# Performance work log

Measured on AMD Instinct MI355X. Metric: run time of the kernel, lower is better.

The kernel has to match this reference:

```python
import jax, jax.numpy as jnp
import numpy as np

DT = 10.0 / 200  # 0.05
DX = 20.0 / 128  # 0.15625

# 5x5 fixed finite-difference stencils (torch Conv2d = cross-correlation, so use as-is)
_LAPL = np.array([[0, 0, -1/12, 0, 0],
                  [0, 0,  4/3,  0, 0],
                  [-1/12, 4/3, -5, 4/3, -1/12],
                  [0, 0,  4/3,  0, 0],
                  [0, 0, -1/12, 0, 0]], dtype=np.float32)
_PAR_X = np.array([[0, 0,  1/12, 0, 0],
                   [0, 0, -8/12, 0, 0],
                   [0, 0,  0,    0, 0],
                   [0, 0,  8/12, 0, 0],
                   [0, 0, -1/12, 0, 0]], dtype=np.float32)


def _conv2d_valid(x, kern):
    # x: [N, 1, H, W], kern: [5, 5] -> [N, 1, H-4, W-4]
    return jax.lax.conv_general_dilated(x, jnp.asarray(kern)[None, None], (1, 1), 'VALID')


def _time_deriv(x):
    # x: [T, B, 1, h, w]; central diff interior, one-sided at endpoints (all /DT)
    interior = (x[2:] - x[:-2]) / (2.0 * DT)
    t0 = (-1.5 * x[0] + 2.0 * x[1] - 0.5 * x[2]) / DT
    tn = (0.5 * x[-3] - 2.0 * x[-2] + 1.5 * x[-1]) / DT
    return jnp.concatenate([t0[None], interior, tn[None]], axis=0)


def setup_inputs() -> dict:
    key = jax.random.key(0)
    output = jax.random.normal(key, (20, 8, 3, 256, 256), dtype=jnp.float32)
    return {"output": output}


def reference(output):
    T, B, C, H, W = output.shape
    u = output[:, :, 1:2]  # [T,B,1,H,W]
    v = output[:, :, 2:3]

    lap_u = _conv2d_valid(u.reshape(T * B, 1, H, W), _LAPL).reshape(T, B, 1, H - 4, W - 4) / (DX ** 2)
    lap_v = _conv2d_valid(v.reshape(T * B, 1, H, W), _LAPL).reshape(T, B, 1, H - 4, W - 4) / (DX ** 2)

    uc = u[:, :, :, 2:-2, 2:-2]  # [T,B,1,H-4,W-4]
    vc = v[:, :, :, 2:-2, 2:-2]
    u_t = _time_deriv(uc)
    v_t = _time_deriv(vc)

    Du, Dv = 0.16, 0.08
    f, k = 0.06, 0.062
    f_u = Du * lap_u - uc * vc ** 2 + f * (1.0 - uc) - u_t
    f_v = Dv * lap_v + uc * vc ** 2 - (f + k) * vc - v_t
    return (f_u, f_v)
```

## Files before the change

kernel.cpp:

```cpp
#include <hip/hip_runtime.h>


#define T_OUT (8 * 252 * 252)

typedef float vf4 __attribute__((ext_vector_type(4)));

static __device__ __forceinline__ vf4 ldu4(const float* p) {
    vf4 v;
    __builtin_memcpy(&v, p, 16);
    return v;
}

#define GS_INT(c) { \
    float ut = (ucn.c - u_cm1.c) * hdt; \
    float vt = (vcn.c - v_cm1.c) * hdt; \
    float uvv = u_cc.c * v_cc.c * v_cc.c; \
    fu.c = Du * u_lm1.c - uvv + fR * (1.0f - u_cc.c) - ut; \
    fv.c = Dv * v_lm1.c + uvv - (fR + kR) * v_cc.c - vt; }

#define GS_T0(c) { \
    float ut = (-1.5f * u_cm1.c + 2.0f * u_cc.c - 0.5f * ucn.c) * inv_dt; \
    float vt = (-1.5f * v_cm1.c + 2.0f * v_cc.c - 0.5f * vcn.c) * inv_dt; \
    float uvv = u_cm1.c * v_cm1.c * v_cm1.c; \
    fu.c = Du * u_l0.c - uvv + fR * (1.0f - u_cm1.c) - ut; \
    fv.c = Dv * v_l0.c + uvv - (fR + kR) * v_cm1.c - vt; }

#define GS_TN(c) { \
    float ut = (0.5f * u_cm2.c - 2.0f * u_cm1.c + 1.5f * u_cc.c) * inv_dt; \
    float vt = (0.5f * v_cm2.c - 2.0f * v_cm1.c + 1.5f * v_cc.c) * inv_dt; \
    float uvv = u_cc.c * v_cc.c * v_cc.c; \
    fu.c = Du * u_lm1.c - uvv + fR * (1.0f - u_cc.c) - ut; \
    fv.c = Dv * v_lm1.c + uvv - (fR + kR) * v_cc.c - vt; }

__global__ __launch_bounds__(256) void gs_loss_kernel(
    const float* __restrict__ in, float* __restrict__ out)
{
    const int tid  = threadIdx.x;
    const int xg   = tid & 63;
    const int yloc = tid >> 6;
    if (xg >= 63) return;

    const int b     = blockIdx.x & 7;
    const int ytile = blockIdx.x >> 3;

    const int y  = ytile * 4 + yloc;
    const int x0 = xg * 4;

    const int planeStride = 256 * 256;
    const int bStride     = 3 * planeStride;
    const int tStride     = 8 * bStride;

    const float* ubase = in + (size_t)b * bStride + planeStride
                         + (size_t)(y + 2) * 256 + x0;

    const int total = 20 * T_OUT;
    float* outu = out + ((size_t)b * 252 + y) * 252 + x0;
    float* outv = outu + total;

    const float C1 = 4.0f / 3.0f, C2 = 1.0f / 12.0f;
    const float inv_dx2 = 1.0f / (0.15625f * 0.15625f);
    const float inv_dt  = 20.0f;
    const float hdt     = 10.0f;
    const float Du = 0.16f, Dv = 0.08f, fR = 0.06f, kR = 0.062f;

    vf4 u_cm2{}, u_cm1{}, u_cc{}, u_lm1{}, u_l0{};
    vf4 v_cm2{}, v_cm1{}, v_cc{}, v_lm1{}, v_l0{};

    for (int t = 0; t < 20; ++t) {
        const float* up = ubase + (size_t)t * tStride;
        const float* vp = up + planeStride;

        vf4 uL = *(const vf4*)(up);
        vf4 uR = *(const vf4*)(up + 4);
        vf4 um1 = ldu4(up - 256 + 2);
        vf4 up1 = ldu4(up + 256 + 2);
        vf4 um2 = ldu4(up - 512 + 2);
        vf4 up2 = ldu4(up + 512 + 2);

        vf4 vL = *(const vf4*)(vp);
        vf4 vR = *(const vf4*)(vp + 4);
        vf4 vm1 = ldu4(vp - 256 + 2);
        vf4 vp1 = ldu4(vp + 256 + 2);
        vf4 vm2 = ldu4(vp - 512 + 2);
        vf4 vp2 = ldu4(vp + 512 + 2);

        vf4 lu, lv;
        lu.x = (C1*(uL.y + uL.w + um1.x + up1.x) - C2*(uL.x + uR.x + um2.x + up2.x) - 5.0f*uL.z) * inv_dx2;
        lu.y = (C1*(uL.z + uR.x + um1.y + up1.y) - C2*(uL.y + uR.y + um2.y + up2.y) - 5.0f*uL.w) * inv_dx2;
        lu.z = (C1*(uL.w + uR.y + um1.z + up1.z) - C2*(uL.z + uR.z + um2.z + up2.z) - 5.0f*uR.x) * inv_dx2;
        lu.w = (C1*(uR.x + uR.z + um1.w + up1.w) - C2*(uL.w + uR.w + um2.w + up2.w) - 5.0f*uR.y) * inv_dx2;
        lv.x = (C1*(vL.y + vL.w + vm1.x + vp1.x) - C2*(vL.x + vR.x + vm2.x + vp2.x) - 5.0f*vL.z) * inv_dx2;
        lv.y = (C1*(vL.z + vR.x + vm1.y + vp1.y) - C2*(vL.y + vR.y + vm2.y + vp2.y) - 5.0f*vL.w) * inv_dx2;
        lv.z = (C1*(vL.w + vR.y + vm1.z + vp1.z) - C2*(vL.z + vR.z + vm2.z + vp2.z) - 5.0f*vR.x) * inv_dx2;
        lv.w = (C1*(vR.x + vR.z + vm1.w + vp1.w) - C2*(vL.w + vR.w + vm2.w + vp2.w) - 5.0f*vR.y) * inv_dx2;

        vf4 ucn = {uL.z, uL.w, uR.x, uR.y};
        vf4 vcn = {vL.z, vL.w, vR.x, vR.y};

        if (t == 0) { u_l0 = lu; v_l0 = lv; }

        if (t == 2) {
            vf4 fu, fv;
            GS_T0(x); GS_T0(y); GS_T0(z); GS_T0(w);
            __builtin_nontemporal_store(fu, (vf4*)(outu));
            __builtin_nontemporal_store(fv, (vf4*)(outv));
        }

        if (t >= 2) {
            vf4 fu, fv;
            GS_INT(x); GS_INT(y); GS_INT(z); GS_INT(w);
            __builtin_nontemporal_store(fu, (vf4*)(outu + (size_t)(t - 1) * T_OUT));
            __builtin_nontemporal_store(fv, (vf4*)(outv + (size_t)(t - 1) * T_OUT));
        }

        u_cm2 = u_cm1; u_cm1 = u_cc; u_cc = ucn; u_lm1 = lu;
        v_cm2 = v_cm1; v_cm1 = v_cc; v_cc = vcn; v_lm1 = lv;
    }

    {
        vf4 fu, fv;
        GS_TN(x); GS_TN(y); GS_TN(z); GS_TN(w);
        __builtin_nontemporal_store(fu, (vf4*)(outu + (size_t)19 * T_OUT));
        __builtin_nontemporal_store(fv, (vf4*)(outv + (size_t)19 * T_OUT));
    }
}

extern "C" void kernel_launch(void* const* d_in, const int* in_sizes, int n_in,
                              void* d_out, int out_size, void* d_ws, size_t ws_size,
                              hipStream_t stream) {
    const float* in = (const float*)d_in[0];
    float* out = (float*)d_out;

    gs_loss_kernel<<<8 * 63, 256, 0, stream>>>(in, out);
}
```

Baseline: 197.8 us.

## Stage stencil rows through double-buffered LDS with register prefetch of next timestep

```diff
diff --git a/kernel.cpp b/kernel.cpp
--- a/kernel.cpp
+++ b/kernel.cpp
@@ -5,7 +5,7 @@
 
 typedef float vf4 __attribute__((ext_vector_type(4)));
 
-static __device__ __forceinline__ vf4 ldu4(const float* p) {
+static __device__ __forceinline__ vf4 lds4u(const float* p) {
     vf4 v;
     __builtin_memcpy(&v, p, 16);
     return v;
@@ -32,29 +32,40 @@
     fu.c = Du * u_lm1.c - uvv + fR * (1.0f - u_cc.c) - ut; \
     fv.c = Dv * v_lm1.c + uvv - (fR + kR) * v_cc.c - vt; }
 
+#define ISSUE(t) { \
+    const float* bt = base0 + (size_t)(t) * tStride; \
+    sreg0 = *(const vf4*)(bt + (size_t)(y0 + w) * 256 + col); \
+    sreg1 = *(const vf4*)(bt + (size_t)(y0 + w + 4) * 256 + col); \
+    sreg2 = *(const vf4*)(bt + planeStride + (size_t)(y0 + w) * 256 + col); \
+    sreg3 = *(const vf4*)(bt + planeStride + (size_t)(y0 + w + 4) * 256 + col); }
+
 __global__ __launch_bounds__(256) void gs_loss_kernel(
     const float* __restrict__ in, float* __restrict__ out)
 {
-    const int tid  = threadIdx.x;
-    const int xg   = tid & 63;
-    const int yloc = tid >> 6;
-    if (xg >= 63) return;
+    __shared__ float lds[2][16][256];
+
+    const int tid = threadIdx.x;
+    const int w   = tid >> 6;
+    const int ln  = tid & 63;
 
     const int b     = blockIdx.x & 7;
     const int ytile = blockIdx.x >> 3;
-
-    const int y  = ytile * 4 + yloc;
-    const int x0 = xg * 4;
+    const int y0    = ytile * 4;
 
     const int planeStride = 256 * 256;
     const int bStride     = 3 * planeStride;
-    const int tStride     = 8 * bStride;
+    const int tStride     = 24 * planeStride;
 
-    const float* ubase = in + (size_t)b * bStride + planeStride
-                         + (size_t)(y + 2) * 256 + x0;
+    const int col = ln * 4;
+    const float* base0 = in + (size_t)b * bStride + planeStride;
+
+    const int yloc = w;
+    const int xg   = ln;
+    const int x0   = xg * 4;
+    const bool active = (xg < 63);
 
     const int total = 20 * T_OUT;
-    float* outu = out + ((size_t)b * 252 + y) * 252 + x0;
+    float* outu = out + ((size_t)b * 252 + (y0 + yloc)) * 252 + x0;
     float* outv = outu + total;
 
     const float C1 = 4.0f / 3.0f, C2 = 1.0f / 12.0f;
@@ -66,58 +77,72 @@
     vf4 u_cm2{}, u_cm1{}, u_cc{}, u_lm1{}, u_l0{};
     vf4 v_cm2{}, v_cm1{}, v_cc{}, v_lm1{}, v_l0{};
 
+    vf4 sreg0, sreg1, sreg2, sreg3;
+    ISSUE(0);
+
+#pragma unroll
     for (int t = 0; t < 20; ++t) {
-        const float* up = ubase + (size_t)t * tStride;
-        const float* vp = up + planeStride;
+        float (*L)[256] = lds[t & 1];
 
-        vf4 uL = *(const vf4*)(up);
-        vf4 uR = *(const vf4*)(up + 4);
-        vf4 um1 = ldu4(up - 256 + 2);
-        vf4 up1 = ldu4(up + 256 + 2);
-        vf4 um2 = ldu4(up - 512 + 2);
-        vf4 up2 = ldu4(up + 512 + 2);
+        *(vf4*)&L[w     ][col] = sreg0;
+        *(vf4*)&L[w + 4 ][col] = sreg1;
+        *(vf4*)&L[w + 8 ][col] = sreg2;
+        *(vf4*)&L[w + 12][col] = sreg3;
 
-        vf4 vL = *(const vf4*)(vp);
-        vf4 vR = *(const vf4*)(vp + 4);
-        vf4 vm1 = ldu4(vp - 256 + 2);
-        vf4 vp1 = ldu4(vp + 256 + 2);
-        vf4 vm2 = ldu4(vp - 512 + 2);
-        vf4 vp2 = ldu4(vp + 512 + 2);
+        __syncthreads();
 
-        vf4 lu, lv;
-        lu.x = (C1*(uL.y + uL.w + um1.x + up1.x) - C2*(uL.x + uR.x + um2.x + up2.x) - 5.0f*uL.z) * inv_dx2;
-        lu.y = (C1*(uL.z + uR.x + um1.y + up1.y) - C2*(uL.y + uR.y + um2.y + up2.y) - 5.0f*uL.w) * inv_dx2;
-        lu.z = (C1*(uL.w + uR.y + um1.z + up1.z) - C2*(uL.z + uR.z + um2.z + up2.z) - 5.0f*uR.x) * inv_dx2;
-        lu.w = (C1*(uR.x + uR.z + um1.w + up1.w) - C2*(uL.w + uR.w + um2.w + up2.w) - 5.0f*uR.y) * inv_dx2;
-        lv.x = (C1*(vL.y + vL.w + vm1.x + vp1.x) - C2*(vL.x + vR.x + vm2.x + vp2.x) - 5.0f*vL.z) * inv_dx2;
-        lv.y = (C1*(vL.z + vR.x + vm1.y + vp1.y) - C2*(vL.y + vR.y + vm2.y + vp2.y) - 5.0f*vL.w) * inv_dx2;
-        lv.z = (C1*(vL.w + vR.y + vm1.z + vp1.z) - C2*(vL.z + vR.z + vm2.z + vp2.z) - 5.0f*vR.x) * inv_dx2;
-        lv.w = (C1*(vR.x + vR.z + vm1.w + vp1.w) - C2*(vL.w + vR.w + vm2.w + vp2.w) - 5.0f*vR.y) * inv_dx2;
+        if (t < 19) ISSUE(t + 1);
 
-        vf4 ucn = {uL.z, uL.w, uR.x, uR.y};
-        vf4 vcn = {vL.z, vL.w, vR.x, vR.y};
+        if (active) {
+            vf4 uL  = *(const vf4*)&L[yloc + 2][x0];
+            vf4 uR  = *(const vf4*)&L[yloc + 2][x0 + 4];
+            vf4 um1 = lds4u(&L[yloc + 1][x0 + 2]);
+            vf4 up1 = lds4u(&L[yloc + 3][x0 + 2]);
+            vf4 um2 = lds4u(&L[yloc    ][x0 + 2]);
+            vf4 up2 = lds4u(&L[yloc + 4][x0 + 2]);
 
-        if (t == 0) { u_l0 = lu; v_l0 = lv; }
+            vf4 vL  = *(const vf4*)&L[yloc + 10][x0];
+            vf4 vR  = *(const vf4*)&L[yloc + 10][x0 + 4];
+            vf4 vm1 = lds4u(&L[yloc +  9][x0 + 2]);
+            vf4 vp1 = lds4u(&L[yloc + 11][x0 + 2]);
+            vf4 vm2 = lds4u(&L[yloc +  8][x0 + 2]);
+            vf4 vp2 = lds4u(&L[yloc + 12][x0 + 2]);
 
-        if (t == 2) {
-            vf4 fu, fv;
-            GS_T0(x); GS_T0(y); GS_T0(z); GS_T0(w);
-            __builtin_nontemporal_store(fu, (vf4*)(outu));
-            __builtin_nontemporal_store(fv, (vf4*)(outv));
+            vf4 lu, lv;
+            lu.x = (C1*(uL.y + uL.w + um1.x + up1.x) - C2*(uL.x + uR.x + um2.x + up2.x) - 5.0f*uL.z) * inv_dx2;
+            lu.y = (C1*(uL.z + uR.x + um1.y + up1.y) - C2*(uL.y + uR.y + um2.y + up2.y) - 5.0f*uL.w) * inv_dx2;
+            lu.z = (C1*(uL.w + uR.y + um1.z + up1.z) - C2*(uL.z + uR.z + um2.z + up2.z) - 5.0f*uR.x) * inv_dx2;
+            lu.w = (C1*(uR.x + uR.z + um1.w + up1.w) - C2*(uL.w + uR.w + um2.w + up2.w) - 5.0f*uR.y) * inv_dx2;
+            lv.x = (C1*(vL.y + vL.w + vm1.x + vp1.x) - C2*(vL.x + vR.x + vm2.x + vp2.x) - 5.0f*vL.z) * inv_dx2;
+            lv.y = (C1*(vL.z + vR.x + vm1.y + vp1.y) - C2*(vL.y + vR.y + vm2.y + vp2.y) - 5.0f*vL.w) * inv_dx2;
+            lv.z = (C1*(vL.w + vR.y + vm1.z + vp1.z) - C2*(vL.z + vR.z + vm2.z + vp2.z) - 5.0f*vR.x) * inv_dx2;
+            lv.w = (C1*(vR.x + vR.z + vm1.w + vp1.w) - C2*(vL.w + vR.w + vm2.w + vp2.w) - 5.0f*vR.y) * inv_dx2;
+
+            vf4 ucn = {uL.z, uL.w, uR.x, uR.y};
+            vf4 vcn = {vL.z, vL.w, vR.x, vR.y};
+
+            if (t == 0) { u_l0 = lu; v_l0 = lv; }
+
+            if (t == 2) {
+                vf4 fu, fv;
+                GS_T0(x); GS_T0(y); GS_T0(z); GS_T0(w);
+                __builtin_nontemporal_store(fu, (vf4*)(outu));
+                __builtin_nontemporal_store(fv, (vf4*)(outv));
+            }
+
+            if (t >= 2) {
+                vf4 fu, fv;
+                GS_INT(x); GS_INT(y); GS_INT(z); GS_INT(w);
+                __builtin_nontemporal_store(fu, (vf4*)(outu + (size_t)(t - 1) * T_OUT));
+                __builtin_nontemporal_store(fv, (vf4*)(outv + (size_t)(t - 1) * T_OUT));
+            }
+
+            u_cm2 = u_cm1; u_cm1 = u_cc; u_cc = ucn; u_lm1 = lu;
+            v_cm2 = v_cm1; v_cm1 = v_cc; v_cc = vcn; v_lm1 = lv;
         }
-
-        if (t >= 2) {
-            vf4 fu, fv;
-            GS_INT(x); GS_INT(y); GS_INT(z); GS_INT(w);
-            __builtin_nontemporal_store(fu, (vf4*)(outu + (size_t)(t - 1) * T_OUT));
-            __builtin_nontemporal_store(fv, (vf4*)(outv + (size_t)(t - 1) * T_OUT));
-        }
-
-        u_cm2 = u_cm1; u_cm1 = u_cc; u_cc = ucn; u_lm1 = lu;
-        v_cm2 = v_cm1; v_cm1 = v_cc; v_cc = vcn; v_lm1 = lv;
     }
 
-    {
+    if (active) {
         vf4 fu, fv;
         GS_TN(x); GS_TN(y); GS_TN(z); GS_TN(w);
         __builtin_nontemporal_store(fu, (vf4*)(outu + (size_t)19 * T_OUT));
```

New measurement: 191.0 us. 1.04x faster.
